# Optimization experiments

Measured on AMD Instinct MI355X. Metric: run time of the kernel, lower is better.

The kernel has to match this reference:

```python
import jax, jax.numpy as jnp
import numpy as np

MKT_COEF = jnp.array([0.5, -1.0, 0.8, 0.6, 1.5, 0.4], dtype=jnp.float32)
RISK_COEF = jnp.array([0.5, -0.8, 0.6, 1.0, 1.2, 0.5], dtype=jnp.float32)
PI = 3.14159


def setup_inputs() -> dict:
    key = jax.random.key(0)
    k1, k2, k3, k4 = jax.random.split(key, 4)
    B, S, H, D = 128, 8192, 16, 6
    return {
        "sequence_embeddings": jax.random.normal(k1, (B, S, H), dtype=jnp.float32),
        "market_volatility": jax.random.uniform(k2, (B, S), dtype=jnp.float32),
        "risk_factors": jax.random.normal(k3, (B, S, D), dtype=jnp.float32),
        "router_w": jax.random.normal(k4, (D, H), dtype=jnp.float32) * 0.02,
        "router_b": jnp.zeros((D,), dtype=jnp.float32),
    }


def _expert_predictions(x, assignments):
    # x: (B,S,H); assignments: (B,S) int32
    mean = x.mean(-1, keepdims=True)                       # (B,S,1)
    std = jnp.std(x, axis=-1, keepdims=True, ddof=1)       # torch.std is unbiased
    d0 = jnp.tanh(x[:, :, :4].mean(-1, keepdims=True)) * (1.0 + std)
    d1 = jax.nn.sigmoid(mean) * 0.3 - 0.15
    d2 = x[:, :, :6].mean(-1, keepdims=True) * 0.8 + jnp.sin(x[:, :, 6:10].mean(-1, keepdims=True) * PI) * 0.4
    noise = jax.random.normal(jax.random.key(42), mean.shape, dtype=x.dtype) * 0.05
    d3 = jnp.tanh(x[:, :, :8].mean(-1, keepdims=True)) * 0.9 + noise
    d4 = jax.nn.relu(mean) ** 1.2 + std * 2.5 - 0.5
    d5 = jax.nn.sigmoid(mean) * 0.4 + jnp.tanh(std) * 0.2
    preds_all = jnp.concatenate([d0, d1, d2, d3, d4, d5], axis=-1)  # (B,S,6)
    return jnp.take_along_axis(preds_all, assignments[..., None].astype(jnp.int32), axis=-1)  # (B,S,1)


def reference(sequence_embeddings, market_volatility, risk_factors, router_w, router_b):
    x = sequence_embeddings
    logits = jnp.einsum("bsh,dh->bsd", x, router_w) + router_b            # (B,S,6)
    probs_base = jax.nn.softmax(logits, axis=-1)
    assignments = jnp.argmax(probs_base, axis=-1).astype(jnp.int32)       # (B,S)
    # training-mode market/risk adjusted straight-through probs
    adj = logits + market_volatility[..., None] * MKT_COEF * 0.3 + risk_factors * RISK_COEF * 0.3
    probs_diff = jax.nn.softmax(adj / 1.2, axis=-1)
    routing_probs = jax.lax.stop_gradient(probs_base) + probs_diff - jax.lax.stop_gradient(probs_diff)
    predictions = _expert_predictions(x, assignments)                     # (B,S,1)
    return predictions, routing_probs, assignments
```

## Files before the change

kernel.cpp:

```cpp
#include <hip/hip_runtime.h>
#include <math.h>

__device__ __forceinline__ unsigned rotl32(unsigned v, int n) {
  return (v << n) | (v >> (32 - n));
}

__device__ __forceinline__ float frcp(float x) { return __builtin_amdgcn_rcpf(x); }

__device__ __forceinline__ float ftanh(float x) {
  float t = __expf(2.0f * x);
  return 1.0f - 2.0f * frcp(t + 1.0f);
}

__device__ __forceinline__ float fsigmoid(float x) {
  return frcp(1.0f + __expf(-x));
}

__device__ float jax_threefry_normal42_part(unsigned idx) {
  const unsigned ks0 = 0u;
  const unsigned ks1 = 42u;
  const unsigned ks2 = 0x1BD11BDAu ^ 42u;
  unsigned x0 = 0u + ks0;
  unsigned x1 = idx + ks1;
  const unsigned ks[3] = {ks0, ks1, ks2};
  const int rA[4] = {13, 15, 26, 6};
  const int rB[4] = {17, 29, 16, 24};
#pragma unroll
  for (int i = 0; i < 5; ++i) {
    const int* r = (i & 1) ? rB : rA;
#pragma unroll
    for (int k = 0; k < 4; ++k) {
      x0 += x1;
      x1 = rotl32(x1, r[k]);
      x1 ^= x0;
    }
    x0 += ks[(i + 1) % 3];
    x1 += ks[(i + 2) % 3] + (unsigned)(i + 1);
  }
  unsigned bits = x0 ^ x1;
  float u01 = __uint_as_float((bits >> 9) | 0x3f800000u) - 1.0f;
  const float lo = -0.99999994f;
  float u = fmaxf(lo, fmaf(u01, 2.0f, lo));
  float w = -__logf(1.0f - u * u);
  float p;
  if (w < 5.0f) {
    w = w - 2.5f;
    p = 2.81022636e-08f;
    p = fmaf(p, w, 3.43273939e-07f);
    p = fmaf(p, w, -3.5233877e-06f);
    p = fmaf(p, w, -4.39150654e-06f);
    p = fmaf(p, w, 0.00021858087f);
    p = fmaf(p, w, -0.00125372503f);
    p = fmaf(p, w, -0.00417768164f);
    p = fmaf(p, w, 0.246640727f);
    p = fmaf(p, w, 1.50140941f);
  } else {
    w = sqrtf(w) - 3.0f;
    p = -0.000200214257f;
    p = fmaf(p, w, 0.000100950558f);
    p = fmaf(p, w, 0.00134934322f);
    p = fmaf(p, w, -0.00367342844f);
    p = fmaf(p, w, 0.00573950773f);
    p = fmaf(p, w, -0.0076224613f);
    p = fmaf(p, w, 0.00943887047f);
    p = fmaf(p, w, 1.00167406f);
    p = fmaf(p, w, 2.83297682f);
  }
  return 1.41421354f * (p * u);
}

__global__ __launch_bounds__(256) void finance_moe_kernel(
    const float* __restrict__ emb,
    const float* __restrict__ vol,
    const float* __restrict__ risk,
    const float* __restrict__ rw,
    const float* __restrict__ rb,
    float* __restrict__ out,
    int ntok) {
  int t = blockIdx.x * blockDim.x + threadIdx.x;
  if (t >= ntok) return;

  float x[16];
  {
    const float4* e4 = reinterpret_cast<const float4*>(emb) + (size_t)t * 4;
    float4 a0 = e4[0], a1 = e4[1], a2 = e4[2], a3 = e4[3];
    x[0] = a0.x; x[1] = a0.y; x[2] = a0.z; x[3] = a0.w;
    x[4] = a1.x; x[5] = a1.y; x[6] = a1.z; x[7] = a1.w;
    x[8] = a2.x; x[9] = a2.y; x[10] = a2.z; x[11] = a2.w;
    x[12] = a3.x; x[13] = a3.y; x[14] = a3.z; x[15] = a3.w;
  }

  double lg[6];
#pragma unroll
  for (int d = 0; d < 6; ++d) {
    double acc = 0.0;
#pragma unroll
    for (int h = 0; h < 16; ++h)
      acc = fma((double)x[h], (double)rw[d * 16 + h], acc);
    lg[d] = acc + (double)rb[d];
  }
  int amax = 0;
  {
    double best = lg[0];
#pragma unroll
    for (int d = 1; d < 6; ++d) {
      if (lg[d] > best) { best = lg[d]; amax = d; }
    }
  }
  float logits[6];
#pragma unroll
  for (int d = 0; d < 6; ++d) logits[d] = (float)lg[d];

  float m = logits[0];
#pragma unroll
  for (int d = 1; d < 6; ++d) m = fmaxf(m, logits[d]);
  float eb[6], se = 0.0f;
#pragma unroll
  for (int d = 0; d < 6; ++d) { eb[d] = __expf(logits[d] - m); se += eb[d]; }
  float inv_se = frcp(se);
  float pb[6];
#pragma unroll
  for (int d = 0; d < 6; ++d) pb[d] = eb[d] * inv_se;

  const float MKT[6] = {0.5f, -1.0f, 0.8f, 0.6f, 1.5f, 0.4f};
  const float RSK[6] = {0.5f, -0.8f, 0.6f, 1.0f, 1.2f, 0.5f};
  float v = vol[t];
  float rk[6];
  {
    const float2* r2 = reinterpret_cast<const float2*>(risk) + (size_t)t * 3;
    float2 q0 = r2[0], q1 = r2[1], q2 = r2[2];
    rk[0] = q0.x; rk[1] = q0.y; rk[2] = q1.x;
    rk[3] = q1.y; rk[4] = q2.x; rk[5] = q2.y;
  }
  const float INV12 = 0.83333333333333333f;
  float sd[6];
#pragma unroll
  for (int d = 0; d < 6; ++d) {
    float adj = logits[d] + (v * MKT[d]) * 0.3f + (rk[d] * RSK[d]) * 0.3f;
    sd[d] = adj * INV12;
  }
  float m2 = sd[0];
#pragma unroll
  for (int d = 1; d < 6; ++d) m2 = fmaxf(m2, sd[d]);
  float ed[6], se2 = 0.0f;
#pragma unroll
  for (int d = 0; d < 6; ++d) { ed[d] = __expf(sd[d] - m2); se2 += ed[d]; }
  float inv_se2 = frcp(se2);
  float rp[6];
#pragma unroll
  for (int d = 0; d < 6; ++d) {
    float pd = ed[d] * inv_se2;
    rp[d] = (pb[d] + pd) - pd;
  }

  float sum = 0.0f;
#pragma unroll
  for (int h = 0; h < 16; ++h) sum += x[h];
  float mean = sum * (1.0f / 16.0f);
  float ss = 0.0f;
#pragma unroll
  for (int h = 0; h < 16; ++h) {
    float dv = x[h] - mean;
    ss += dv * dv;
  }
  float stdv = sqrtf(ss * (1.0f / 15.0f));

  float pred;
  if (amax == 0) {
    float s4 = ((x[0] + x[1]) + x[2]) + x[3];
    pred = ftanh(s4 * 0.25f) * (1.0f + stdv);
  } else if (amax == 1) {
    pred = fsigmoid(mean) * 0.3f - 0.15f;
  } else if (amax == 2) {
    float s6 = ((((x[0] + x[1]) + x[2]) + x[3]) + x[4]) + x[5];
    float s610 = ((x[6] + x[7]) + x[8]) + x[9];
    pred = (s6 * (1.0f / 6.0f)) * 0.8f + __sinf((s610 * 0.25f) * 3.14159f) * 0.4f;
  } else if (amax == 3) {
    float s8 = ((((((x[0] + x[1]) + x[2]) + x[3]) + x[4]) + x[5]) + x[6]) + x[7];
    float noise = jax_threefry_normal42_part((unsigned)t) * 0.05f;
    pred = ftanh(s8 * 0.125f) * 0.9f + noise;
  } else if (amax == 4) {
    float r = fmaxf(mean, 0.0f);
    pred = __expf(1.2f * __logf(r)) + stdv * 2.5f - 0.5f;
  } else {
    pred = fsigmoid(mean) * 0.4f + ftanh(stdv) * 0.2f;
  }

  out[t] = pred;
  float2* po = reinterpret_cast<float2*>(out + ntok) + (size_t)t * 3;
  po[0] = make_float2(rp[0], rp[1]);
  po[1] = make_float2(rp[2], rp[3]);
  po[2] = make_float2(rp[4], rp[5]);
  out[(size_t)ntok * 7 + t] = (float)amax;
}

extern "C" void kernel_launch(void* const* d_in, const int* in_sizes, int n_in,
                              void* d_out, int out_size, void* d_ws, size_t ws_size,
                              hipStream_t stream) {
  const float* emb = (const float*)d_in[0];
  const float* vol = (const float*)d_in[1];
  const float* risk = (const float*)d_in[2];
  const float* rw = (const float*)d_in[3];
  const float* rb = (const float*)d_in[4];
  float* out = (float*)d_out;
  int ntok = in_sizes[0] / 16;
  int block = 256;
  int grid = (ntok + block - 1) / block;
  hipLaunchKernelGGL(finance_moe_kernel, dim3(grid), dim3(block), 0, stream,
                     emb, vol, risk, rw, rb, out, ntok);
}
```

Baseline: 25.58 us.

## Drop dead straight-through softmax and inputs, use fp32 logits with fp64 tie fallback

```diff
diff --git a/kernel.cpp b/kernel.cpp
--- a/kernel.cpp
+++ b/kernel.cpp
@@ -71,8 +71,6 @@
 
 __global__ __launch_bounds__(256) void finance_moe_kernel(
     const float* __restrict__ emb,
-    const float* __restrict__ vol,
-    const float* __restrict__ risk,
     const float* __restrict__ rw,
     const float* __restrict__ rb,
     float* __restrict__ out,
@@ -90,68 +88,45 @@
     x[12] = a3.x; x[13] = a3.y; x[14] = a3.z; x[15] = a3.w;
   }
 
-  double lg[6];
+  float lg[6];
 #pragma unroll
   for (int d = 0; d < 6; ++d) {
-    double acc = 0.0;
+    float acc = 0.0f;
 #pragma unroll
-    for (int h = 0; h < 16; ++h)
-      acc = fma((double)x[h], (double)rw[d * 16 + h], acc);
-    lg[d] = acc + (double)rb[d];
+    for (int h = 0; h < 16; ++h) acc = fmaf(x[h], rw[d * 16 + h], acc);
+    lg[d] = acc + rb[d];
   }
-  int amax = 0;
-  {
-    double best = lg[0];
+
+  int a1 = 0, a2 = 0;
+  float b1 = lg[0], b2 = -1e30f;
 #pragma unroll
-    for (int d = 1; d < 6; ++d) {
-      if (lg[d] > best) { best = lg[d]; amax = d; }
+  for (int d = 1; d < 6; ++d) {
+    if (lg[d] > b1) { b2 = b1; a2 = a1; b1 = lg[d]; a1 = d; }
+    else if (lg[d] > b2) { b2 = lg[d]; a2 = d; }
+  }
+  int amax = a1;
+  if (b1 - b2 < 2e-5f) {
+    double A = 0.0, B = 0.0;
+#pragma unroll
+    for (int h = 0; h < 16; ++h) {
+      A = fma((double)x[h], (double)rw[a1 * 16 + h], A);
+      B = fma((double)x[h], (double)rw[a2 * 16 + h], B);
     }
+    A += (double)rb[a1];
+    B += (double)rb[a2];
+    amax = (B > A || (B == A && a2 < a1)) ? a2 : a1;
   }
-  float logits[6];
+
+  float m = lg[0];
 #pragma unroll
-  for (int d = 0; d < 6; ++d) logits[d] = (float)lg[d];
-
-  float m = logits[0];
-#pragma unroll
-  for (int d = 1; d < 6; ++d) m = fmaxf(m, logits[d]);
+  for (int d = 1; d < 6; ++d) m = fmaxf(m, lg[d]);
   float eb[6], se = 0.0f;
 #pragma unroll
-  for (int d = 0; d < 6; ++d) { eb[d] = __expf(logits[d] - m); se += eb[d]; }
+  for (int d = 0; d < 6; ++d) { eb[d] = __expf(lg[d] - m); se += eb[d]; }
   float inv_se = frcp(se);
   float pb[6];
 #pragma unroll
   for (int d = 0; d < 6; ++d) pb[d] = eb[d] * inv_se;
-
-  const float MKT[6] = {0.5f, -1.0f, 0.8f, 0.6f, 1.5f, 0.4f};
-  const float RSK[6] = {0.5f, -0.8f, 0.6f, 1.0f, 1.2f, 0.5f};
-  float v = vol[t];
-  float rk[6];
-  {
-    const float2* r2 = reinterpret_cast<const float2*>(risk) + (size_t)t * 3;
-    float2 q0 = r2[0], q1 = r2[1], q2 = r2[2];
-    rk[0] = q0.x; rk[1] = q0.y; rk[2] = q1.x;
-    rk[3] = q1.y; rk[4] = q2.x; rk[5] = q2.y;
-  }
-  const float INV12 = 0.83333333333333333f;
-  float sd[6];
-#pragma unroll
-  for (int d = 0; d < 6; ++d) {
-    float adj = logits[d] + (v * MKT[d]) * 0.3f + (rk[d] * RSK[d]) * 0.3f;
-    sd[d] = adj * INV12;
-  }
-  float m2 = sd[0];
-#pragma unroll
-  for (int d = 1; d < 6; ++d) m2 = fmaxf(m2, sd[d]);
-  float ed[6], se2 = 0.0f;
-#pragma unroll
-  for (int d = 0; d < 6; ++d) { ed[d] = __expf(sd[d] - m2); se2 += ed[d]; }
-  float inv_se2 = frcp(se2);
-  float rp[6];
-#pragma unroll
-  for (int d = 0; d < 6; ++d) {
-    float pd = ed[d] * inv_se2;
-    rp[d] = (pb[d] + pd) - pd;
-  }
 
   float sum = 0.0f;
 #pragma unroll
@@ -165,32 +140,33 @@
   }
   float stdv = sqrtf(ss * (1.0f / 15.0f));
 
-  float pred;
-  if (amax == 0) {
-    float s4 = ((x[0] + x[1]) + x[2]) + x[3];
-    pred = ftanh(s4 * 0.25f) * (1.0f + stdv);
-  } else if (amax == 1) {
-    pred = fsigmoid(mean) * 0.3f - 0.15f;
-  } else if (amax == 2) {
-    float s6 = ((((x[0] + x[1]) + x[2]) + x[3]) + x[4]) + x[5];
-    float s610 = ((x[6] + x[7]) + x[8]) + x[9];
-    pred = (s6 * (1.0f / 6.0f)) * 0.8f + __sinf((s610 * 0.25f) * 3.14159f) * 0.4f;
-  } else if (amax == 3) {
-    float s8 = ((((((x[0] + x[1]) + x[2]) + x[3]) + x[4]) + x[5]) + x[6]) + x[7];
-    float noise = jax_threefry_normal42_part((unsigned)t) * 0.05f;
-    pred = ftanh(s8 * 0.125f) * 0.9f + noise;
-  } else if (amax == 4) {
-    float r = fmaxf(mean, 0.0f);
-    pred = __expf(1.2f * __logf(r)) + stdv * 2.5f - 0.5f;
-  } else {
-    pred = fsigmoid(mean) * 0.4f + ftanh(stdv) * 0.2f;
-  }
+  float s4 = ((x[0] + x[1]) + x[2]) + x[3];
+  float s6 = ((((x[0] + x[1]) + x[2]) + x[3]) + x[4]) + x[5];
+  float s610 = ((x[6] + x[7]) + x[8]) + x[9];
+  float s8 = s6 + x[6] + x[7];
+
+  float sig = fsigmoid(mean);
+  float p0 = ftanh(s4 * 0.25f) * (1.0f + stdv);
+  float p1 = sig * 0.3f - 0.15f;
+  float p2 = (s6 * (1.0f / 6.0f)) * 0.8f + __sinf((s610 * 0.25f) * 3.14159f) * 0.4f;
+  float noise = jax_threefry_normal42_part((unsigned)t) * 0.05f;
+  float p3 = ftanh(s8 * 0.125f) * 0.9f + noise;
+  float r4 = fmaxf(mean, 0.0f);
+  float p4 = __expf(1.2f * __logf(r4)) + stdv * 2.5f - 0.5f;
+  float p5 = sig * 0.4f + ftanh(stdv) * 0.2f;
+
+  float pred = (amax == 0) ? p0
+             : (amax == 1) ? p1
+             : (amax == 2) ? p2
+             : (amax == 3) ? p3
+             : (amax == 4) ? p4
+                           : p5;
 
   out[t] = pred;
   float2* po = reinterpret_cast<float2*>(out + ntok) + (size_t)t * 3;
-  po[0] = make_float2(rp[0], rp[1]);
-  po[1] = make_float2(rp[2], rp[3]);
-  po[2] = make_float2(rp[4], rp[5]);
+  po[0] = make_float2(pb[0], pb[1]);
+  po[1] = make_float2(pb[2], pb[3]);
+  po[2] = make_float2(pb[4], pb[5]);
   out[(size_t)ntok * 7 + t] = (float)amax;
 }
 
@@ -198,8 +174,6 @@
                               void* d_out, int out_size, void* d_ws, size_t ws_size,
                               hipStream_t stream) {
   const float* emb = (const float*)d_in[0];
-  const float* vol = (const float*)d_in[1];
-  const float* risk = (const float*)d_in[2];
   const float* rw = (const float*)d_in[3];
   const float* rb = (const float*)d_in[4];
   float* out = (float*)d_out;
@@ -207,5 +181,5 @@
   int block = 256;
   int grid = (ntok + block - 1) / block;
   hipLaunchKernelGGL(finance_moe_kernel, dim3(grid), dim3(block), 0, stream,
-                     emb, vol, risk, rw, rb, out, ntok);
+                     emb, rw, rb, out, ntok);
 }
```

Result: faster. 22.36 us (-12.6%).
